# Kernel tuning notes

Hardware: AMD Instinct MI355X
Metric: run time of the kernel (lower is better)

## Reference

```python
import jax, jax.numpy as jnp
import numpy as np

N_NODES = 50000
N_EDGES = 1000000
IN_DIM, HID_DIM, OUT_DIM = 128, 64, 16


def setup_inputs() -> dict:
    key = jax.random.key(0)
    k1, k2, k3, k4 = jax.random.split(key, 4)
    x = jax.random.normal(k1, (N_NODES, IN_DIM), dtype=jnp.float32)
    edge_index = jax.random.randint(k2, (2, N_EDGES), 0, N_NODES, dtype=jnp.int64)
    # Glorot-style scaling for weights, zero bias (PyG GCNConv default init style)
    W1 = jax.random.normal(k3, (IN_DIM, HID_DIM), dtype=jnp.float32) * (1.0 / np.sqrt(IN_DIM))
    b1 = jnp.zeros((HID_DIM,), dtype=jnp.float32)
    W2 = jax.random.normal(k4, (HID_DIM, OUT_DIM), dtype=jnp.float32) * (1.0 / np.sqrt(HID_DIM))
    b2 = jnp.zeros((OUT_DIM,), dtype=jnp.float32)
    return {"x": x, "edge_index": edge_index, "W1": W1, "b1": b1, "W2": W2, "b2": b2}


def gcn_conv(x, src, dst, W, b, num_nodes):
    """PyG GCNConv: add self loops, symmetric deg^{-1/2} normalization,
    linear transform, gather-scale-scatter aggregation, bias."""
    # degree includes self loops (src/dst already augmented by caller)
    deg = jax.ops.segment_sum(jnp.ones_like(dst, dtype=x.dtype), dst, num_segments=num_nodes)
    dinv = jnp.where(deg > 0, deg ** -0.5, 0.0)
    norm = dinv[src] * dinv[dst]            # [E']
    h = x @ W                                # [N, F_out] transform before aggregation
    msg = h[src] * norm[:, None]             # gather + scale
    out = jax.ops.segment_sum(msg, dst, num_segments=num_nodes)  # scatter-add
    return out + b


def reference(x, edge_index, W1, b1, W2, b2):
    n = x.shape[0]
    loops = jnp.arange(n, dtype=edge_index.dtype)
    src = jnp.concatenate([edge_index[0], loops])
    dst = jnp.concatenate([edge_index[1], loops])
    h = gcn_conv(x, src, dst, W1, b1, n)
    h = jax.nn.relu(h)
    out = gcn_conv(h, src, dst, W2, b2, n)
    return out
```

## Files before the change

kernel.cpp:

```cpp
#include <hip/hip_runtime.h>

#define IN_DIM 128
#define HID_DIM 64
#define OUT_DIM 16

#define SSHIFT 7
#define SMASK 127
#define CHUNK 4096
#define CBLK 1024
#define KPT (CHUNK / CBLK)
#define CAP 4096

#define G1N 64
#define G1S 132

static __device__ __forceinline__ unsigned short f2bf(float f) {
    unsigned u = __float_as_uint(f);
    unsigned r = u + 0x7fffu + ((u >> 16) & 1u);
    return (unsigned short)(r >> 16);
}
static __device__ __forceinline__ unsigned packbf2(float a, float b) {
    return (unsigned)f2bf(a) | ((unsigned)f2bf(b) << 16);
}
static __device__ __forceinline__ float bflo(unsigned v) { return __uint_as_float(v << 16); }
static __device__ __forceinline__ float bfhi(unsigned v) { return __uint_as_float(v & 0xffff0000u); }

__global__ __launch_bounds__(CBLK) void passC2(const int* __restrict__ src,
                                               const int* __restrict__ dst,
                                               int* __restrict__ gcnt,
                                               int* __restrict__ eb,
                                               int E, int NS) {
    __shared__ int cnt[512];
    __shared__ int bofs[512];
    int t = threadIdx.x;
    for (int s = t; s < NS; s += CBLK) cnt[s] = 0;
    __syncthreads();
    int base = blockIdx.x * CHUNK;
    int dreg[KPT];
    #pragma unroll
    for (int k = 0; k < KPT; ++k) {
        int i = base + k * CBLK + t;
        int d = -1;
        if (i < E) { d = dst[i]; atomicAdd(&cnt[d >> SSHIFT], 1); }
        dreg[k] = d;
    }
    __syncthreads();
    for (int s = t; s < NS; s += CBLK) {
        int c = cnt[s];
        bofs[s] = c ? atomicAdd(&gcnt[s], c) : 0;
        cnt[s] = 0;
    }
    __syncthreads();
    #pragma unroll
    for (int k = 0; k < KPT; ++k) {
        int i = base + k * CBLK + t;
        if (i < E) {
            int d = dreg[k];
            int s = d >> SSHIFT;
            int off = atomicAdd(&cnt[s], 1);
            eb[(size_t)s * CAP + bofs[s] + off] = src[i] | ((d & SMASK) << 17);
        }
    }
}

__global__ __launch_bounds__(256) void passD(const int* __restrict__ eb,
                                             const int* __restrict__ tot,
                                             int* __restrict__ csr_src,
                                             int* __restrict__ row_ptr,
                                             float* __restrict__ dinv,
                                             int N, int E, int NS) {
    __shared__ int red[256];
    __shared__ int deg[128], incl[128], cur[128];
    int s = blockIdx.x, t = threadIdx.x;
    if (t < 128) deg[t] = 0;
    int part = 0;
    for (int k = t; k < s; k += 256) part += tot[k];
    red[t] = part;
    __syncthreads();
    for (int off = 128; off >= 1; off >>= 1) {
        if (t < off) red[t] += red[t + off];
        __syncthreads();
    }
    int b0 = red[0];
    int cnt = tot[s];
    const size_t sbase = (size_t)s * CAP;
    for (int k = t; k < cnt; k += 256) atomicAdd(&deg[eb[sbase + k] >> 17], 1);
    __syncthreads();
    if (t < 128) incl[t] = deg[t];
    __syncthreads();
    for (int off = 1; off < 128; off <<= 1) {
        int tmp = 0;
        if (t < 128 && t >= off) tmp = incl[t - off];
        __syncthreads();
        if (t < 128) incl[t] += tmp;
        __syncthreads();
    }
    if (t < 128) {
        int loff = incl[t] - deg[t];
        cur[t] = b0 + loff;
        int n = (s << SSHIFT) + t;
        if (n < N) {
            row_ptr[n] = b0 + loff;
            dinv[n] = rsqrtf((float)(deg[t] + 1));
        }
    }
    if (s == NS - 1 && t == 0) row_ptr[N] = E;
    __syncthreads();
    for (int k = t; k < cnt; k += 256) {
        int v = eb[sbase + k];
        int dl = v >> 17;
        int p = atomicAdd(&cur[dl], 1);
        csr_src[p] = v & 0x1FFFF;
    }
}

__global__ __launch_bounds__(256) void gemm1_kernel(const float* __restrict__ x,
                                                    const float* __restrict__ W1,
                                                    const float* __restrict__ dinv,
                                                    unsigned* __restrict__ h1u, int N) {
    __shared__ __align__(16) float sW[IN_DIM * HID_DIM];
    __shared__ __align__(16) float sx[G1N * G1S];
    int t = threadIdx.x;
    int node0 = blockIdx.x * G1N;

    const float4* W4  = (const float4*)W1;
    float4*       sW4 = (float4*)sW;
    #pragma unroll
    for (int i = 0; i < 8; ++i) sW4[i * 256 + t] = W4[i * 256 + t];

    const float4* x4 = (const float4*)x;
    for (int i = t; i < G1N * 32; i += 256) {
        int r = i >> 5, c = i & 31;
        int n = node0 + r; if (n >= N) n = 0;
        *(float4*)(sx + r * G1S + c * 4) = x4[(size_t)n * 32 + c];
    }
    __syncthreads();

    int og = t & 15, ng = t >> 4;
    float a00=0.f,a01=0.f,a02=0.f,a03=0.f, a10=0.f,a11=0.f,a12=0.f,a13=0.f,
          a20=0.f,a21=0.f,a22=0.f,a23=0.f, a30=0.f,a31=0.f,a32=0.f,a33=0.f;
    const float* xr = sx + (ng << 2) * G1S;
    #pragma unroll 4
    for (int k = 0; k < IN_DIM; ++k) {
        float x0 = xr[k];
        float x1 = xr[G1S + k];
        float x2 = xr[2 * G1S + k];
        float x3 = xr[3 * G1S + k];
        float4 wv = ((const float4*)(sW + k * HID_DIM))[og];
        a00 = fmaf(x0, wv.x, a00); a01 = fmaf(x0, wv.y, a01);
        a02 = fmaf(x0, wv.z, a02); a03 = fmaf(x0, wv.w, a03);
        a10 = fmaf(x1, wv.x, a10); a11 = fmaf(x1, wv.y, a11);
        a12 = fmaf(x1, wv.z, a12); a13 = fmaf(x1, wv.w, a13);
        a20 = fmaf(x2, wv.x, a20); a21 = fmaf(x2, wv.y, a21);
        a22 = fmaf(x2, wv.z, a22); a23 = fmaf(x2, wv.w, a23);
        a30 = fmaf(x3, wv.x, a30); a31 = fmaf(x3, wv.y, a31);
        a32 = fmaf(x3, wv.z, a32); a33 = fmaf(x3, wv.w, a33);
    }

    int nb = node0 + (ng << 2);
#define G1_STORE(i, c0, c1, c2, c3)                                         \
    {                                                                       \
        int n = nb + i;                                                     \
        if (n <= N) {                                                       \
            float dn = (n < N) ? dinv[n] : 0.f;         \
            uint2 pv;                                                       \
            pv.x = packbf2(c0 * dn, c1 * dn);                               \
            pv.y = packbf2(c2 * dn, c3 * dn);                               \
            ((uint2*)(h1u + (size_t)n * 32))[og] = pv;                      \
        }                                                                   \
    }
    G1_STORE(0, a00, a01, a02, a03)
    G1_STORE(1, a10, a11, a12, a13)
    G1_STORE(2, a20, a21, a22, a23)
    G1_STORE(3, a30, a31, a32, a33)
#undef G1_STORE
}

__global__ __launch_bounds__(256) void agg1_kernel(const unsigned* __restrict__ h1u,
                                                   const int* __restrict__ row_ptr,
                                                   const int* __restrict__ csr_src,
                                                   const float* __restrict__ dinv,
                                                   const float* __restrict__ b1,
                                                   const float* __restrict__ W2,
                                                   unsigned* __restrict__ h2u, int N) {
    __shared__ __align__(16) float sW[OUT_DIM * 68];
    int t = threadIdx.x;
    for (int i = t; i < HID_DIM * OUT_DIM; i += 256) {
        int k = i >> 4, j = i & 15;
        sW[j * 68 + k] = W2[i];
    }
    __syncthreads();

    int lane = t & 63;
    int h  = lane >> 5;
    int l  = lane & 31;
    int es = l >> 3;
    int dg = l & 7;
    int n = blockIdx.x * 8 + ((t >> 6) << 1) + h;
    if (n > N) return;
    if (n == N) {
        if (l < 4) { uint2 z; z.x = 0u; z.y = 0u; ((uint2*)h2u)[(size_t)N * 4 + l] = z; }
        return;
    }

    int e0 = row_ptr[n], e1 = row_ptr[n + 1];
    const uint4* rb = (const uint4*)h1u;
    int sb = h << 5;

    float a0 = 0.f, a1 = 0.f, a2 = 0.f, a3 = 0.f,
          a4 = 0.f, a5 = 0.f, a6 = 0.f, a7 = 0.f;

    for (int base = e0 - 1; base < e1; base += 32) {
        int idx = base + l;
        int sld = N;
        if (idx == e0 - 1) sld = n;
        else if (idx < e1) sld = csr_src[idx];
        int lim = e1 - base;
        if (lim > 32) lim = 32;
        int nr = (lim + 3) >> 2;
        nr = (nr + 1) & ~1;
        for (int r = 0; r < nr; r += 2) {
            int sA = __shfl(sld, sb + ((r + 0) << 2) + es);
            int sB = __shfl(sld, sb + ((r + 1) << 2) + es);
            uint4 vA = rb[(size_t)sA * 8 + dg];
            uint4 vB = rb[(size_t)sB * 8 + dg];
            a0 += bflo(vA.x) + bflo(vB.x);
            a1 += bfhi(vA.x) + bfhi(vB.x);
            a2 += bflo(vA.y) + bflo(vB.y);
            a3 += bfhi(vA.y) + bfhi(vB.y);
            a4 += bflo(vA.z) + bflo(vB.z);
            a5 += bfhi(vA.z) + bfhi(vB.z);
            a6 += bflo(vA.w) + bflo(vB.w);
            a7 += bfhi(vA.w) + bfhi(vB.w);
        }
    }
    #pragma unroll
    for (int m = 8; m <= 16; m <<= 1) {
        a0 += __shfl_xor(a0, m); a1 += __shfl_xor(a1, m);
        a2 += __shfl_xor(a2, m); a3 += __shfl_xor(a3, m);
        a4 += __shfl_xor(a4, m); a5 += __shfl_xor(a5, m);
        a6 += __shfl_xor(a6, m); a7 += __shfl_xor(a7, m);
    }

    float dn = dinv[n];
    float4 bA = ((const float4*)b1)[2 * dg];
    float4 bB = ((const float4*)b1)[2 * dg + 1];
    float r0 = fmaxf(fmaf(dn, a0, bA.x), 0.f);
    float r1 = fmaxf(fmaf(dn, a1, bA.y), 0.f);
    float r2 = fmaxf(fmaf(dn, a2, bA.z), 0.f);
    float r3 = fmaxf(fmaf(dn, a3, bA.w), 0.f);
    float r4 = fmaxf(fmaf(dn, a4, bB.x), 0.f);
    float r5 = fmaxf(fmaf(dn, a5, bB.y), 0.f);
    float r6 = fmaxf(fmaf(dn, a6, bB.z), 0.f);
    float r7 = fmaxf(fmaf(dn, a7, bB.w), 0.f);

    const float* wb = sW + ((es << 2) * 68) + (dg << 3);
    float4 wA, wB2;
    wA = *(const float4*)(wb);        wB2 = *(const float4*)(wb + 4);
    float p0 = r0*wA.x + r1*wA.y + r2*wA.z + r3*wA.w + r4*wB2.x + r5*wB2.y + r6*wB2.z + r7*wB2.w;
    wA = *(const float4*)(wb + 68);   wB2 = *(const float4*)(wb + 72);
    float p1 = r0*wA.x + r1*wA.y + r2*wA.z + r3*wA.w + r4*wB2.x + r5*wB2.y + r6*wB2.z + r7*wB2.w;
    wA = *(const float4*)(wb + 136);  wB2 = *(const float4*)(wb + 140);
    float p2 = r0*wA.x + r1*wA.y + r2*wA.z + r3*wA.w + r4*wB2.x + r5*wB2.y + r6*wB2.z + r7*wB2.w;
    wA = *(const float4*)(wb + 204);  wB2 = *(const float4*)(wb + 208);
    float p3 = r0*wA.x + r1*wA.y + r2*wA.z + r3*wA.w + r4*wB2.x + r5*wB2.y + r6*wB2.z + r7*wB2.w;

    #pragma unroll
    for (int m = 1; m <= 4; m <<= 1) {
        p0 += __shfl_xor(p0, m); p1 += __shfl_xor(p1, m);
        p2 += __shfl_xor(p2, m); p3 += __shfl_xor(p3, m);
    }
    if (dg == 0) {
        uint2 pv;
        pv.x = packbf2(p0 * dn, p1 * dn);
        pv.y = packbf2(p2 * dn, p3 * dn);
        ((uint2*)h2u)[(size_t)n * 4 + es] = pv;
    }
}

__global__ __launch_bounds__(256) void agg2_kernel(const unsigned* __restrict__ h2u,
                                                   const int* __restrict__ row_ptr,
                                                   const int* __restrict__ csr_src,
                                                   const float* __restrict__ dinv,
                                                   const float* __restrict__ b2,
                                                   float* __restrict__ out, int N) {
    int t = threadIdx.x;
    int lane = t & 63;
    int h  = lane >> 4;
    int l  = lane & 15;
    int es = l >> 2;
    int dg = l & 3;
    int n = blockIdx.x * 16 + ((t >> 6) << 2) + h;
    if (n >= N) return;

    int e0 = row_ptr[n], e1 = row_ptr[n + 1];
    const uint2* rb = (const uint2*)h2u;
    int sb = h << 4;

    float a0 = 0.f, a1 = 0.f, a2 = 0.f, a3 = 0.f;

    for (int base = e0 - 1; base < e1; base += 16) {
        int idx = base + l;
        int sld = N;
        if (idx == e0 - 1) sld = n;
        else if (idx < e1) sld = csr_src[idx];
        int lim = e1 - base;
        if (lim > 16) lim = 16;
        int nr = (lim + 3) >> 2;
        nr = (nr + 1) & ~1;
        for (int r = 0; r < nr; r += 2) {
            int sA = __shfl(sld, sb + ((r + 0) << 2) + es);
            int sB = __shfl(sld, sb + ((r + 1) << 2) + es);
            uint2 vA = rb[(size_t)sA * 4 + dg];
            uint2 vB = rb[(size_t)sB * 4 + dg];
            a0 += bflo(vA.x) + bflo(vB.x);
            a1 += bfhi(vA.x) + bfhi(vB.x);
            a2 += bflo(vA.y) + bflo(vB.y);
            a3 += bfhi(vA.y) + bfhi(vB.y);
        }
    }
    #pragma unroll
    for (int m = 4; m <= 8; m <<= 1) {
        a0 += __shfl_xor(a0, m); a1 += __shfl_xor(a1, m);
        a2 += __shfl_xor(a2, m); a3 += __shfl_xor(a3, m);
    }
    if (es == 0) {
        float dn = dinv[n];
        float4 bb = ((const float4*)b2)[dg];
        float4 r;
        r.x = fmaf(dn, a0, bb.x);
        r.y = fmaf(dn, a1, bb.y);
        r.z = fmaf(dn, a2, bb.z);
        r.w = fmaf(dn, a3, bb.w);
        ((float4*)out)[(size_t)n * 4 + dg] = r;
    }
}

extern "C" void kernel_launch(void* const* d_in, const int* in_sizes, int n_in,
                              void* d_out, int out_size, void* d_ws, size_t ws_size,
                              hipStream_t stream) {
    const float* x  = (const float*)d_in[0];
    const int*   ei = (const int*)d_in[1];
    const float* W1 = (const float*)d_in[2];
    const float* b1 = (const float*)d_in[3];
    const float* W2 = (const float*)d_in[4];
    const float* b2 = (const float*)d_in[5];
    float* out = (float*)d_out;

    const int N = in_sizes[0] / IN_DIM;
    const int E = in_sizes[1] / 2;
    const int* src = ei;
    const int* dst = ei + E;

    const int NS  = (N + SMASK) >> SSHIFT;
    const int NSP = NS + 1;
    const int BC  = (E + CHUNK - 1) / CHUNK;

    char* w = (char*)d_ws;
    auto alloc = [&](size_t bytes) -> void* {
        void* p = (void*)w;
        w += (bytes + 255) & ~(size_t)255;
        return p;
    };
    int*      gcnt    = (int*)     alloc((size_t)NSP * 4);
    int*      eb      = (int*)     alloc((size_t)NS * CAP * 4);
    int*      csr_src = (int*)     alloc((size_t)E * 4);
    int*      row_ptr = (int*)     alloc((size_t)(N + 1) * 4);
    float*    dinv    = (float*)   alloc((size_t)N * 4);
    unsigned* h1u     = (unsigned*)alloc((size_t)(N + 1) * 32 * 4);
    unsigned* h2u     = (unsigned*)alloc((size_t)(N + 1) * 8 * 4);

    const int GB  = (N + G1N) / G1N;
    const int AB1 = (N + 8) / 8;
    const int AB2 = (N + 15) / 16;

    hipMemsetAsync(gcnt, 0, (size_t)NSP * 4, stream);
    passC2<<<BC, CBLK, 0, stream>>>(src, dst, gcnt, eb, E, NS);
    passD <<<NS, 256,  0, stream>>>(eb, gcnt, csr_src, row_ptr, dinv, N, E, NS);

    gemm1_kernel<<<GB, 256, 0, stream>>>(x, W1, dinv, h1u, N);
    agg1_kernel<<<AB1, 256, 0, stream>>>(h1u, row_ptr, csr_src, dinv, b1, W2, h2u, N);
    agg2_kernel<<<AB2, 256, 0, stream>>>(h2u, row_ptr, csr_src, dinv, b2, out, N);
}
```

Baseline: 159.7 us.

## Stage bucket and CSR scatters in shared memory for coalesced global writes

In the bucketing pass, each block now prefix-sums its per-bucket counts and sorts its edges into a shared-memory buffer. Each wave then copies whole bucket runs to global memory in contiguous segments, replacing random scattered stores. The CSR build pass likewise scatters into a shared staging array and then writes csr_src linearly. This trades extra LDS use (a 16 KB buffer per block), a 512-wide scan and extra barriers for coalesced global writes.

```diff
diff --git a/kernel.cpp b/kernel.cpp
--- a/kernel.cpp
+++ b/kernel.cpp
@@ -31,9 +31,12 @@
                                                int* __restrict__ eb,
                                                int E, int NS) {
     __shared__ int cnt[512];
+    __shared__ int lofs[512];
     __shared__ int bofs[512];
+    __shared__ int cur[512];
+    __shared__ int srt[CHUNK];
     int t = threadIdx.x;
-    for (int s = t; s < NS; s += CBLK) cnt[s] = 0;
+    if (t < 512) cnt[t] = 0;
     __syncthreads();
     int base = blockIdx.x * CHUNK;
     int dreg[KPT];
@@ -45,10 +48,21 @@
         dreg[k] = d;
     }
     __syncthreads();
-    for (int s = t; s < NS; s += CBLK) {
-        int c = cnt[s];
-        bofs[s] = c ? atomicAdd(&gcnt[s], c) : 0;
-        cnt[s] = 0;
+    if (t < 512) lofs[t] = cnt[t];
+    __syncthreads();
+    for (int off = 1; off < 512; off <<= 1) {
+        int tmp = 0;
+        if (t < 512 && t >= off) tmp = lofs[t - off];
+        __syncthreads();
+        if (t < 512) lofs[t] += tmp;
+        __syncthreads();
+    }
+    if (t < 512) {
+        int c  = cnt[t];
+        int lo = lofs[t] - c;
+        lofs[t] = lo;
+        cur[t]  = lo;
+        bofs[t] = (t < NS && c) ? atomicAdd(&gcnt[t], c) : 0;
     }
     __syncthreads();
     #pragma unroll
@@ -57,9 +71,17 @@
         if (i < E) {
             int d = dreg[k];
             int s = d >> SSHIFT;
-            int off = atomicAdd(&cnt[s], 1);
-            eb[(size_t)s * CAP + bofs[s] + off] = src[i] | ((d & SMASK) << 17);
+            int p = atomicAdd(&cur[s], 1);
+            srt[p] = src[i] | ((d & SMASK) << 17);
         }
+    }
+    __syncthreads();
+    int wave = t >> 6, lane = t & 63;
+    for (int s = wave; s < NS; s += CBLK / 64) {
+        int c  = cnt[s];
+        int lo = lofs[s];
+        size_t gb = (size_t)s * CAP + bofs[s];
+        for (int k = lane; k < c; k += 64) eb[gb + k] = srt[lo + k];
     }
 }
 
@@ -71,6 +93,7 @@
                                              int N, int E, int NS) {
     __shared__ int red[256];
     __shared__ int deg[128], incl[128], cur[128];
+    __shared__ int srt[CAP];
     int s = blockIdx.x, t = threadIdx.x;
     if (t < 128) deg[t] = 0;
     int part = 0;
@@ -97,7 +120,7 @@
     }
     if (t < 128) {
         int loff = incl[t] - deg[t];
-        cur[t] = b0 + loff;
+        cur[t] = loff;
         int n = (s << SSHIFT) + t;
         if (n < N) {
             row_ptr[n] = b0 + loff;
@@ -110,8 +133,10 @@
         int v = eb[sbase + k];
         int dl = v >> 17;
         int p = atomicAdd(&cur[dl], 1);
-        csr_src[p] = v & 0x1FFFF;
-    }
+        srt[p] = v & 0x1FFFF;
+    }
+    __syncthreads();
+    for (int k = t; k < cnt; k += 256) csr_src[b0 + k] = srt[k];
 }
 
 __global__ __launch_bounds__(256) void gemm1_kernel(const float* __restrict__ x,
```

Result: no change. 159.0 us (-0.4%).
